# Performance work log

Hardware: AMD Instinct MI355X
Metric: run time of the kernel (lower is better)

Reference implementation:

```python
import jax, jax.numpy as jnp
import numpy as np

D = 1024  # input_size
H = 1024  # hidden_size
B = 128
R = 512


def _lin(x, W, b):
    return x @ W + b


def setup_inputs() -> dict:
    key = jax.random.key(0)
    ks = jax.random.split(key, 20)
    s = 0.02
    inp = {
        "V": jax.random.normal(ks[0], (B, R, D), jnp.float32),
        "s_t": jax.random.normal(ks[1], (B, D), jnp.float32),
        "h_t": jax.random.normal(ks[2], (B, D), jnp.float32),
        # weights stored [in, out] (y = x @ W + b)
        "Wv": jax.random.normal(ks[3], (D, H), jnp.float32) * s,
        "bv": jnp.zeros((H,), jnp.float32),
        "Wsp": jax.random.normal(ks[4], (D, D), jnp.float32) * s,
        "bsp": jnp.zeros((D,), jnp.float32),
        "Wsa": jax.random.normal(ks[5], (D, H), jnp.float32) * s,
        "bsa": jnp.zeros((H,), jnp.float32),
        "Whp": jax.random.normal(ks[6], (D, D), jnp.float32) * s,
        "bhp": jnp.zeros((D,), jnp.float32),
        "Wha": jax.random.normal(ks[7], (D, H), jnp.float32) * s,
        "bha": jnp.zeros((H,), jnp.float32),
        "Wal": jax.random.normal(ks[8], (H, 1), jnp.float32) * s,
        "bal": jnp.zeros((1,), jnp.float32),
        "Wcp": jax.random.normal(ks[9], (D, D), jnp.float32) * s,
        "bcp": jnp.zeros((D,), jnp.float32),
    }
    return inp


def reference(V, s_t, h_t, Wv, bv, Wsp, bsp, Wsa, bsa, Whp, bhp, Wha, bha, Wal, bal, Wcp, bcp):
    v_embed = jax.nn.relu(_lin(V, Wv, bv))           # [B,R,H]
    s_proj = jax.nn.relu(_lin(s_t, Wsp, bsp))        # [B,D]
    s_att = _lin(s_proj, Wsa, bsa)                   # [B,H]
    h_proj = jnp.tanh(_lin(h_t, Whp, bhp))           # [B,D]
    h_att = _lin(h_proj, Wha, bha)                   # [B,H]
    regions = jnp.concatenate([V, s_proj[:, None, :]], axis=1)           # [B,R+1,D]
    regions_att = jnp.concatenate([v_embed, s_att[:, None, :]], axis=1)  # [B,R+1,H]
    alpha_input = jnp.tanh(regions_att + h_att[:, None, :])              # [B,R+1,H]
    scores = (_lin(alpha_input, Wal, bal)).squeeze(-1)                   # [B,R+1]
    alpha = jax.nn.softmax(scores, axis=1)                               # [B,R+1]
    context = jnp.einsum("br,brd->bd", alpha, regions)                   # [B,D]
    z_t = jnp.tanh(_lin(context + h_proj, Wcp, bcp))                     # [B,D]
    return z_t
```

## Files before the change

kernel.cpp:

```cpp
#include <hip/hip_runtime.h>


typedef __bf16 bf16x8 __attribute__((ext_vector_type(8)));
typedef float floatx4 __attribute__((ext_vector_type(4)));

__device__ __forceinline__ float tanh_fast(float x) {
    x = fminf(10.0f, fmaxf(-10.0f, x));
    float e = exp2f(x * 2.885390081777927f);
    return (e - 1.0f) * __builtin_amdgcn_rcpf(e + 1.0f);
}

__global__ __launch_bounds__(256) void wvt_kernel(
    const float* __restrict__ Wv, __bf16* __restrict__ WvT) {
    __shared__ float tile[64][65];
    const int k0 = blockIdx.x * 64, n0 = blockIdx.y * 64;
    const int c = threadIdx.x & 63, r = threadIdx.x >> 6;
#pragma unroll
    for (int i = 0; i < 16; ++i)
        tile[r + i * 4][c] = Wv[(size_t)(k0 + r + i * 4) * 1024 + n0 + c];
    __syncthreads();
#pragma unroll
    for (int i = 0; i < 16; ++i)
        WvT[(size_t)(n0 + r + i * 4) * 1024 + k0 + c] =
            (__bf16)tile[c][r + i * 4];
}

__global__ __launch_bounds__(512) void small_gemm_k(
    const float* __restrict__ A0, const float* __restrict__ W0,
    const float* __restrict__ b0, float* __restrict__ C0, int act0,
    const float* __restrict__ A1, const float* __restrict__ W1,
    const float* __restrict__ b1, float* __restrict__ C1, int act1) {
    const float* A; const float* W; const float* bs; float* C; int act;
    if (blockIdx.z == 0) { A = A0; W = W0; bs = b0; C = C0; act = act0; }
    else                 { A = A1; W = W1; bs = b1; C = C1; act = act1; }
    __shared__ float red[3][8][128];
    const int tid = threadIdx.x;
    const int nl = tid & 127, kq = tid >> 7;
    const int n = blockIdx.x * 128 + nl;
    const int m0 = blockIdx.y * 8;
    const float* Ab = A + m0 * 1024;
    float acc[8] = {};
    const int kbeg = kq * 256, kend = kbeg + 256;
#pragma unroll 4
    for (int k = kbeg; k < kend; ++k) {
        float w = W[(size_t)k * 1024 + n];
#pragma unroll
        for (int mi = 0; mi < 8; ++mi)
            acc[mi] = fmaf(Ab[mi * 1024 + k], w, acc[mi]);
    }
    if (kq > 0) {
#pragma unroll
        for (int mi = 0; mi < 8; ++mi) red[kq - 1][mi][nl] = acc[mi];
    }
    __syncthreads();
    if (kq == 0) {
        float bias = bs[n];
#pragma unroll
        for (int mi = 0; mi < 8; ++mi) {
            float v = acc[mi] + red[0][mi][nl] + red[1][mi][nl] +
                      red[2][mi][nl] + bias;
            if (act == 1) v = fmaxf(v, 0.0f);
            else if (act == 2) v = tanh_fast(v);
            C[(size_t)(m0 + mi) * 1024 + n] = v;
        }
    }
}

__global__ __launch_bounds__(256, 3) void score_gemm_k(
    const float* __restrict__ V, const __bf16* __restrict__ WvT,
    const float* __restrict__ bv, const float* __restrict__ h_att,
    const float* __restrict__ Wal, float* __restrict__ scores) {
    __shared__ __bf16 As[2][128 * 40];
    __shared__ __bf16 Bs[2][128 * 32];

    const int tid = threadIdx.x;
    const int bid = blockIdx.x;
    const int xcd = bid & 7;
    const int j = bid >> 3;
    const int mtile = xcd * 64 + (j >> 3);
    const int ntile = j & 7;
    const int m0 = mtile * 128, n0 = ntile * 128;
    const int wid = tid >> 6, lane = tid & 63;
    const int wm = wid & 1, wn = wid >> 1;
    const int lcol = lane & 15, quad = lane >> 4;

    floatx4 acc[4][4] = {};

    const int am = tid >> 1;
    const int ak = (tid & 1) * 16;
    const float* aptr = V + (size_t)(m0 + am) * 1024 + ak;

    const int g0n = tid >> 2, g0ks = tid & 3;
    const int g1n = (256 + tid) >> 2, g1ks = tid & 3;
    const int g0kg = g0ks ^ ((g0n >> 1) & 3);
    const int g1kg = g1ks ^ ((g1n >> 1) & 3);
    const __bf16* bp0 = WvT + (size_t)(n0 + g0n) * 1024 + g0kg * 8;
    const __bf16* bp1 = WvT + (size_t)(n0 + g1n) * 1024 + g1kg * 8;

    auto stage_A = [&](int buf, float4 f0, float4 f1, float4 f2, float4 f3) {
        bf16x8 u0, u1;
        u0[0] = (__bf16)f0.x; u0[1] = (__bf16)f0.y;
        u0[2] = (__bf16)f0.z; u0[3] = (__bf16)f0.w;
        u0[4] = (__bf16)f1.x; u0[5] = (__bf16)f1.y;
        u0[6] = (__bf16)f1.z; u0[7] = (__bf16)f1.w;
        u1[0] = (__bf16)f2.x; u1[1] = (__bf16)f2.y;
        u1[2] = (__bf16)f2.z; u1[3] = (__bf16)f2.w;
        u1[4] = (__bf16)f3.x; u1[5] = (__bf16)f3.y;
        u1[6] = (__bf16)f3.z; u1[7] = (__bf16)f3.w;
        __bf16* awr = &As[buf][am * 40 + ak];
        *reinterpret_cast<bf16x8*>(awr) = u0;
        *reinterpret_cast<bf16x8*>(awr + 8) = u1;
    };
    auto dma_B = [&](int buf, int k0) {
        __builtin_amdgcn_global_load_lds(
            (const __attribute__((address_space(1))) void*)(bp0 + k0),
            (__attribute__((address_space(3))) void*)(&Bs[buf][tid * 8]),
            16, 0, 0);
        __builtin_amdgcn_global_load_lds(
            (const __attribute__((address_space(1))) void*)(bp1 + k0),
            (__attribute__((address_space(3))) void*)(&Bs[buf][(256 + tid) * 8]),
            16, 0, 0);
    };

    dma_B(0, 0);
    {
        const float4* fp = reinterpret_cast<const float4*>(aptr);
        stage_A(0, fp[0], fp[1], fp[2], fp[3]);
    }
    __syncthreads();

    for (int kk = 0; kk < 32; ++kk) {
        const int cur = kk & 1, nxt = cur ^ 1;
        float4 f0, f1, f2, f3;
        const bool pf = (kk < 31);
        if (pf) {
            dma_B(nxt, (kk + 1) * 32);
            const float4* fp =
                reinterpret_cast<const float4*>(aptr + (kk + 1) * 32);
            f0 = fp[0]; f1 = fp[1]; f2 = fp[2]; f3 = fp[3];
        }
        bf16x8 af[4], bfr[4];
#pragma unroll
        for (int mi = 0; mi < 4; ++mi)
            af[mi] = *reinterpret_cast<const bf16x8*>(
                &As[cur][(wm * 64 + mi * 16 + lcol) * 40 + quad * 8]);
#pragma unroll
        for (int ni = 0; ni < 4; ++ni) {
            int n = wn * 64 + ni * 16 + lcol;
            int ks = quad ^ ((n >> 1) & 3);
            bfr[ni] = *reinterpret_cast<const bf16x8*>(
                &Bs[cur][n * 32 + ks * 8]);
        }
#pragma unroll
        for (int mi = 0; mi < 4; ++mi)
#pragma unroll
            for (int ni = 0; ni < 4; ++ni)
                acc[mi][ni] = __builtin_amdgcn_mfma_f32_16x16x32_bf16(
                    af[mi], bfr[ni], acc[mi][ni], 0, 0, 0);
        if (pf) stage_A(nxt, f0, f1, f2, f3);
        __syncthreads();
    }

    const int b = m0 >> 9;
    float wal[4], hat[4], bvv[4];
#pragma unroll
    for (int ni = 0; ni < 4; ++ni) {
        int n = n0 + wn * 64 + ni * 16 + lcol;
        wal[ni] = Wal[n];
        hat[ni] = h_att[b * 1024 + n];
        bvv[ni] = bv[n];
    }
    float p[16];
#pragma unroll
    for (int mi = 0; mi < 4; ++mi) {
#pragma unroll
        for (int rg = 0; rg < 4; ++rg) {
            float s = 0.f;
#pragma unroll
            for (int ni = 0; ni < 4; ++ni) {
                float x = acc[mi][ni][rg] + bvv[ni];
                x = fmaxf(x, 0.f);
                s = fmaf(wal[ni], tanh_fast(x + hat[ni]), s);
            }
            p[mi * 4 + rg] = s;
        }
    }
#pragma unroll
    for (int off = 1; off < 16; off <<= 1) {
#pragma unroll
        for (int i = 0; i < 16; ++i) p[i] += __shfl_xor(p[i], off, 64);
    }
    if (lcol == 0) {
#pragma unroll
        for (int mi = 0; mi < 4; ++mi)
#pragma unroll
            for (int rg = 0; rg < 4; ++rg) {
                int row = m0 + wm * 64 + mi * 16 + quad * 4 + rg;
                atomicAdd(&scores[b * 513 + (row & 511)], p[mi * 4 + rg]);
            }
    }
}

__global__ __launch_bounds__(256) void lastrow_k(
    const float* __restrict__ s_att, const float* __restrict__ h_att,
    const float* __restrict__ Wal, float* __restrict__ scores) {
    int b = blockIdx.x, tid = threadIdx.x;
    float s = 0.f;
    for (int h = tid; h < 1024; h += 256)
        s += Wal[h] * tanh_fast(s_att[b * 1024 + h] + h_att[b * 1024 + h]);
#pragma unroll
    for (int off = 32; off >= 1; off >>= 1) s += __shfl_xor(s, off, 64);
    __shared__ float red[4];
    if ((tid & 63) == 0) red[tid >> 6] = s;
    __syncthreads();
    if (tid == 0) scores[b * 513 + 512] = red[0] + red[1] + red[2] + red[3];
}

__global__ __launch_bounds__(256) void softmax_k(
    const float* __restrict__ scores, float* __restrict__ alpha) {
    int b = blockIdx.x, tid = threadIdx.x;
    const float* s = scores + b * 513;
    float v0 = s[tid];
    float v1 = s[tid + 256];
    float v2 = (tid == 0) ? s[512] : -1e30f;
    float m = fmaxf(v0, fmaxf(v1, v2));
#pragma unroll
    for (int off = 32; off >= 1; off >>= 1) m = fmaxf(m, __shfl_xor(m, off, 64));
    __shared__ float red[4];
    int w = tid >> 6;
    if ((tid & 63) == 0) red[w] = m;
    __syncthreads();
    m = fmaxf(fmaxf(red[0], red[1]), fmaxf(red[2], red[3]));
    const float L2E = 1.4426950408889634f;
    float e0 = exp2f((v0 - m) * L2E);
    float e1 = exp2f((v1 - m) * L2E);
    float e2 = (tid == 0) ? exp2f((v2 - m) * L2E) : 0.f;
    float sum = e0 + e1 + e2;
#pragma unroll
    for (int off = 32; off >= 1; off >>= 1) sum += __shfl_xor(sum, off, 64);
    __syncthreads();
    if ((tid & 63) == 0) red[w] = sum;
    __syncthreads();
    sum = red[0] + red[1] + red[2] + red[3];
    float inv = 1.0f / sum;
    float* a = alpha + b * 513;
    a[tid] = e0 * inv;
    a[tid + 256] = e1 * inv;
    if (tid == 0) a[512] = e2 * inv;
}

__global__ __launch_bounds__(256) void ctx_k(
    const float* __restrict__ V, const float* __restrict__ alpha,
    const float* __restrict__ s_proj, const float* __restrict__ h_proj,
    float* __restrict__ ctxsum) {
    const int b = blockIdx.x, dq = blockIdx.y;
    const int tid = threadIdx.x;
    const int dl = tid & 63, rq = tid >> 6;
    __shared__ float sal[513];
    __shared__ float red[3][64][4];
    for (int i = tid; i < 513; i += 256) sal[i] = alpha[b * 513 + i];
    __syncthreads();
    const int d0 = dq * 256 + dl * 4;
    const float* vp = V + ((size_t)b * 512 + rq * 128) * 1024 + d0;
    float a0 = 0, a1 = 0, a2 = 0, a3 = 0;
#pragma unroll 8
    for (int r = 0; r < 128; ++r) {
        float al = sal[rq * 128 + r];
        const float4 vv = *reinterpret_cast<const float4*>(vp + (size_t)r * 1024);
        a0 = fmaf(al, vv.x, a0); a1 = fmaf(al, vv.y, a1);
        a2 = fmaf(al, vv.z, a2); a3 = fmaf(al, vv.w, a3);
    }
    if (rq > 0) {
        red[rq - 1][dl][0] = a0; red[rq - 1][dl][1] = a1;
        red[rq - 1][dl][2] = a2; red[rq - 1][dl][3] = a3;
    }
    __syncthreads();
    if (rq == 0) {
#pragma unroll
        for (int q = 0; q < 3; ++q) {
            a0 += red[q][dl][0]; a1 += red[q][dl][1];
            a2 += red[q][dl][2]; a3 += red[q][dl][3];
        }
        float4 sp = *reinterpret_cast<const float4*>(s_proj + b * 1024 + d0);
        float4 hp = *reinterpret_cast<const float4*>(h_proj + b * 1024 + d0);
        float aR = sal[512];
        float4 o;
        o.x = fmaf(aR, sp.x, a0) + hp.x;
        o.y = fmaf(aR, sp.y, a1) + hp.y;
        o.z = fmaf(aR, sp.z, a2) + hp.z;
        o.w = fmaf(aR, sp.w, a3) + hp.w;
        *reinterpret_cast<float4*>(ctxsum + b * 1024 + d0) = o;
    }
}

extern "C" void kernel_launch(void* const* d_in, const int* in_sizes, int n_in,
                              void* d_out, int out_size, void* d_ws,
                              size_t ws_size, hipStream_t stream) {
    const float* V   = (const float*)d_in[0];
    const float* s_t = (const float*)d_in[1];
    const float* h_t = (const float*)d_in[2];
    const float* Wv  = (const float*)d_in[3];
    const float* bv  = (const float*)d_in[4];
    const float* Wsp = (const float*)d_in[5];
    const float* bsp = (const float*)d_in[6];
    const float* Wsa = (const float*)d_in[7];
    const float* bsa = (const float*)d_in[8];
    const float* Whp = (const float*)d_in[9];
    const float* bhp = (const float*)d_in[10];
    const float* Wha = (const float*)d_in[11];
    const float* bha = (const float*)d_in[12];
    const float* Wal = (const float*)d_in[13];
    const float* Wcp = (const float*)d_in[15];
    const float* bcp = (const float*)d_in[16];
    float* out = (float*)d_out;

    char* ws = (char*)d_ws;
    __bf16* WvT   = (__bf16*)(ws + 0);
    float* s_proj = (float*)(ws + 2097152);
    float* h_proj = (float*)(ws + 2621440);
    float* s_att  = (float*)(ws + 3145728);
    float* h_att  = (float*)(ws + 3670016);
    float* scores = (float*)(ws + 4194304);
    float* alpha  = (float*)(ws + 4456960);
    float* ctxsum = (float*)(ws + 4719616);

    hipLaunchKernelGGL(wvt_kernel, dim3(16, 16), dim3(256), 0, stream, Wv, WvT);
    hipLaunchKernelGGL(small_gemm_k, dim3(8, 16, 2), dim3(512), 0, stream,
                       s_t, Wsp, bsp, s_proj, 1,
                       h_t, Whp, bhp, h_proj, 2);
    hipLaunchKernelGGL(small_gemm_k, dim3(8, 16, 2), dim3(512), 0, stream,
                       s_proj, Wsa, bsa, s_att, 0,
                       h_proj, Wha, bha, h_att, 0);
    (void)hipMemsetAsync(scores, 0, 128 * 513 * sizeof(float), stream);
    hipLaunchKernelGGL(score_gemm_k, dim3(4096), dim3(256), 0, stream,
                       V, WvT, bv, h_att, Wal, scores);
    hipLaunchKernelGGL(lastrow_k, dim3(128), dim3(256), 0, stream,
                       s_att, h_att, Wal, scores);
    hipLaunchKernelGGL(softmax_k, dim3(128), dim3(256), 0, stream,
                       scores, alpha);
    hipLaunchKernelGGL(ctx_k, dim3(128, 4), dim3(256), 0, stream,
                       V, alpha, s_proj, h_proj, ctxsum);
    hipLaunchKernelGGL(small_gemm_k, dim3(8, 16, 1), dim3(512), 0, stream,
                       ctxsum, Wcp, bcp, out, 2,
                       ctxsum, Wcp, bcp, out, 2);
}
```

Baseline: 879.0 us.

## Pre-convert V to bf16 and load GEMM operands directly into registers

When the workspace is large enough, a new kernel converts V to bf16 once. The score GEMM and the context reduction then read the half-size copy. The score GEMM drops its LDS staging and barriers: each wave loads its A and B fragments straight from global memory into double-buffered registers and computes a 128x64 tile. The context sum now accumulates from bf16 V, which lowers precision and adds an extra full pass over V for the conversion. Whether the workspace is big enough to take this path is unknown.

```diff
diff --git a/kernel.cpp b/kernel.cpp
--- a/kernel.cpp
+++ b/kernel.cpp
@@ -2,12 +2,26 @@
 
 
 typedef __bf16 bf16x8 __attribute__((ext_vector_type(8)));
+typedef __bf16 bf16x4 __attribute__((ext_vector_type(4)));
 typedef float floatx4 __attribute__((ext_vector_type(4)));
 
 __device__ __forceinline__ float tanh_fast(float x) {
     x = fminf(10.0f, fmaxf(-10.0f, x));
     float e = exp2f(x * 2.885390081777927f);
     return (e - 1.0f) * __builtin_amdgcn_rcpf(e + 1.0f);
+}
+
+__global__ __launch_bounds__(256) void vbf_k(
+    const float* __restrict__ V, __bf16* __restrict__ Vb) {
+    size_t idx = ((size_t)blockIdx.x * 256 + threadIdx.x) * 8;
+    float4 f0 = *reinterpret_cast<const float4*>(V + idx);
+    float4 f1 = *reinterpret_cast<const float4*>(V + idx + 4);
+    bf16x8 u;
+    u[0] = (__bf16)f0.x; u[1] = (__bf16)f0.y;
+    u[2] = (__bf16)f0.z; u[3] = (__bf16)f0.w;
+    u[4] = (__bf16)f1.x; u[5] = (__bf16)f1.y;
+    u[6] = (__bf16)f1.z; u[7] = (__bf16)f1.w;
+    *reinterpret_cast<bf16x8*>(Vb + idx) = u;
 }
 
 __global__ __launch_bounds__(256) void wvt_kernel(
@@ -66,113 +80,89 @@
     }
 }
 
-__global__ __launch_bounds__(256, 3) void score_gemm_k(
-    const float* __restrict__ V, const __bf16* __restrict__ WvT,
+template <bool ABF16>
+__global__ __launch_bounds__(256, 2) void score2_k(
+    const void* __restrict__ Vv, const __bf16* __restrict__ WvT,
     const float* __restrict__ bv, const float* __restrict__ h_att,
     const float* __restrict__ Wal, float* __restrict__ scores) {
-    __shared__ __bf16 As[2][128 * 40];
-    __shared__ __bf16 Bs[2][128 * 32];
-
     const int tid = threadIdx.x;
-    const int bid = blockIdx.x;
-    const int xcd = bid & 7;
-    const int j = bid >> 3;
-    const int mtile = xcd * 64 + (j >> 3);
-    const int ntile = j & 7;
-    const int m0 = mtile * 128, n0 = ntile * 128;
+    const int bidx = blockIdx.x;
+    const int xcd = bidx & 7;
+    const int i = bidx >> 3;
+    const int nt = i & 3;
+    const int mloc = i >> 2;
+    const int m0 = (xcd * 64 + mloc) * 128;
     const int wid = tid >> 6, lane = tid & 63;
-    const int wm = wid & 1, wn = wid >> 1;
+    const int n0 = nt * 256 + wid * 64;
     const int lcol = lane & 15, quad = lane >> 4;
 
-    floatx4 acc[4][4] = {};
-
-    const int am = tid >> 1;
-    const int ak = (tid & 1) * 16;
-    const float* aptr = V + (size_t)(m0 + am) * 1024 + ak;
-
-    const int g0n = tid >> 2, g0ks = tid & 3;
-    const int g1n = (256 + tid) >> 2, g1ks = tid & 3;
-    const int g0kg = g0ks ^ ((g0n >> 1) & 3);
-    const int g1kg = g1ks ^ ((g1n >> 1) & 3);
-    const __bf16* bp0 = WvT + (size_t)(n0 + g0n) * 1024 + g0kg * 8;
-    const __bf16* bp1 = WvT + (size_t)(n0 + g1n) * 1024 + g1kg * 8;
-
-    auto stage_A = [&](int buf, float4 f0, float4 f1, float4 f2, float4 f3) {
-        bf16x8 u0, u1;
-        u0[0] = (__bf16)f0.x; u0[1] = (__bf16)f0.y;
-        u0[2] = (__bf16)f0.z; u0[3] = (__bf16)f0.w;
-        u0[4] = (__bf16)f1.x; u0[5] = (__bf16)f1.y;
-        u0[6] = (__bf16)f1.z; u0[7] = (__bf16)f1.w;
-        u1[0] = (__bf16)f2.x; u1[1] = (__bf16)f2.y;
-        u1[2] = (__bf16)f2.z; u1[3] = (__bf16)f2.w;
-        u1[4] = (__bf16)f3.x; u1[5] = (__bf16)f3.y;
-        u1[6] = (__bf16)f3.z; u1[7] = (__bf16)f3.w;
-        __bf16* awr = &As[buf][am * 40 + ak];
-        *reinterpret_cast<bf16x8*>(awr) = u0;
-        *reinterpret_cast<bf16x8*>(awr + 8) = u1;
+    floatx4 acc[8][4] = {};
+
+    const int laneoff = lcol * 1024 + quad * 8;
+    const __bf16* Ab = (const __bf16*)Vv + (size_t)m0 * 1024 + laneoff;
+    const float* Af = (const float*)Vv + (size_t)m0 * 1024 + laneoff;
+    const __bf16* Bb = WvT + (size_t)n0 * 1024 + laneoff;
+
+    bf16x8 a[2][8], b[2][4];
+
+    auto loadstep = [&](int buf, int kk) {
+        const int ke = kk * 32;
+        if constexpr (ABF16) {
+#pragma unroll
+            for (int mi = 0; mi < 8; ++mi)
+                a[buf][mi] = *reinterpret_cast<const bf16x8*>(
+                    Ab + mi * 16384 + ke);
+        } else {
+#pragma unroll
+            for (int mi = 0; mi < 8; ++mi) {
+                const float* p = Af + mi * 16384 + ke;
+                float4 f0 = *reinterpret_cast<const float4*>(p);
+                float4 f1 = *reinterpret_cast<const float4*>(p + 4);
+                bf16x8 u;
+                u[0] = (__bf16)f0.x; u[1] = (__bf16)f0.y;
+                u[2] = (__bf16)f0.z; u[3] = (__bf16)f0.w;
+                u[4] = (__bf16)f1.x; u[5] = (__bf16)f1.y;
+                u[6] = (__bf16)f1.z; u[7] = (__bf16)f1.w;
+                a[buf][mi] = u;
+            }
+        }
+#pragma unroll
+        for (int ni = 0; ni < 4; ++ni)
+            b[buf][ni] = *reinterpret_cast<const bf16x8*>(
+                Bb + ni * 16384 + ke);
     };
-    auto dma_B = [&](int buf, int k0) {
-        __builtin_amdgcn_global_load_lds(
-            (const __attribute__((address_space(1))) void*)(bp0 + k0),
-            (__attribute__((address_space(3))) void*)(&Bs[buf][tid * 8]),
-            16, 0, 0);
-        __builtin_amdgcn_global_load_lds(
-            (const __attribute__((address_space(1))) void*)(bp1 + k0),
-            (__attribute__((address_space(3))) void*)(&Bs[buf][(256 + tid) * 8]),
-            16, 0, 0);
-    };
-
-    dma_B(0, 0);
-    {
-        const float4* fp = reinterpret_cast<const float4*>(aptr);
-        stage_A(0, fp[0], fp[1], fp[2], fp[3]);
-    }
-    __syncthreads();
-
-    for (int kk = 0; kk < 32; ++kk) {
-        const int cur = kk & 1, nxt = cur ^ 1;
-        float4 f0, f1, f2, f3;
-        const bool pf = (kk < 31);
-        if (pf) {
-            dma_B(nxt, (kk + 1) * 32);
-            const float4* fp =
-                reinterpret_cast<const float4*>(aptr + (kk + 1) * 32);
-            f0 = fp[0]; f1 = fp[1]; f2 = fp[2]; f3 = fp[3];
-        }
-        bf16x8 af[4], bfr[4];
-#pragma unroll
-        for (int mi = 0; mi < 4; ++mi)
-            af[mi] = *reinterpret_cast<const bf16x8*>(
-                &As[cur][(wm * 64 + mi * 16 + lcol) * 40 + quad * 8]);
-#pragma unroll
-        for (int ni = 0; ni < 4; ++ni) {
-            int n = wn * 64 + ni * 16 + lcol;
-            int ks = quad ^ ((n >> 1) & 3);
-            bfr[ni] = *reinterpret_cast<const bf16x8*>(
-                &Bs[cur][n * 32 + ks * 8]);
-        }
-#pragma unroll
-        for (int mi = 0; mi < 4; ++mi)
+    auto mfmastep = [&](int buf) {
+#pragma unroll
+        for (int mi = 0; mi < 8; ++mi)
 #pragma unroll
             for (int ni = 0; ni < 4; ++ni)
                 acc[mi][ni] = __builtin_amdgcn_mfma_f32_16x16x32_bf16(
-                    af[mi], bfr[ni], acc[mi][ni], 0, 0, 0);
-        if (pf) stage_A(nxt, f0, f1, f2, f3);
-        __syncthreads();
-    }
-
-    const int b = m0 >> 9;
+                    a[buf][mi], b[buf][ni], acc[mi][ni], 0, 0, 0);
+    };
+
+    loadstep(0, 0);
+    for (int kk2 = 0; kk2 < 15; ++kk2) {
+        loadstep(1, 2 * kk2 + 1);
+        mfmastep(0);
+        loadstep(0, 2 * kk2 + 2);
+        mfmastep(1);
+    }
+    loadstep(1, 31);
+    mfmastep(0);
+    mfmastep(1);
+
+    const int b_idx = m0 >> 9;
     float wal[4], hat[4], bvv[4];
 #pragma unroll
     for (int ni = 0; ni < 4; ++ni) {
-        int n = n0 + wn * 64 + ni * 16 + lcol;
+        int n = n0 + ni * 16 + lcol;
         wal[ni] = Wal[n];
-        hat[ni] = h_att[b * 1024 + n];
+        hat[ni] = h_att[b_idx * 1024 + n];
         bvv[ni] = bv[n];
     }
-    float p[16];
-#pragma unroll
-    for (int mi = 0; mi < 4; ++mi) {
+    float p[32];
+#pragma unroll
+    for (int mi = 0; mi < 8; ++mi) {
 #pragma unroll
         for (int rg = 0; rg < 4; ++rg) {
             float s = 0.f;
@@ -188,15 +178,16 @@
 #pragma unroll
     for (int off = 1; off < 16; off <<= 1) {
 #pragma unroll
-        for (int i = 0; i < 16; ++i) p[i] += __shfl_xor(p[i], off, 64);
+        for (int j = 0; j < 32; ++j) p[j] += __shfl_xor(p[j], off, 64);
     }
     if (lcol == 0) {
 #pragma unroll
-        for (int mi = 0; mi < 4; ++mi)
+        for (int mi = 0; mi < 8; ++mi)
 #pragma unroll
             for (int rg = 0; rg < 4; ++rg) {
-                int row = m0 + wm * 64 + mi * 16 + quad * 4 + rg;
-                atomicAdd(&scores[b * 513 + (row & 511)], p[mi * 4 + rg]);
+                int row = m0 + mi * 16 + quad * 4 + rg;
+                atomicAdd(&scores[b_idx * 513 + (row & 511)],
+                          p[mi * 4 + rg]);
             }
     }
 }
@@ -249,8 +240,9 @@
     if (tid == 0) a[512] = e2 * inv;
 }
 
-__global__ __launch_bounds__(256) void ctx_k(
-    const float* __restrict__ V, const float* __restrict__ alpha,
+template <bool VBF>
+__global__ __launch_bounds__(256) void ctx2_k(
+    const void* __restrict__ Vv, const float* __restrict__ alpha,
     const float* __restrict__ s_proj, const float* __restrict__ h_proj,
     float* __restrict__ ctxsum) {
     const int b = blockIdx.x, dq = blockIdx.y;
@@ -261,14 +253,31 @@
     for (int i = tid; i < 513; i += 256) sal[i] = alpha[b * 513 + i];
     __syncthreads();
     const int d0 = dq * 256 + dl * 4;
-    const float* vp = V + ((size_t)b * 512 + rq * 128) * 1024 + d0;
     float a0 = 0, a1 = 0, a2 = 0, a3 = 0;
+    if constexpr (VBF) {
+        const __bf16* vp =
+            (const __bf16*)Vv + ((size_t)b * 512 + rq * 128) * 1024 + d0;
 #pragma unroll 8
-    for (int r = 0; r < 128; ++r) {
-        float al = sal[rq * 128 + r];
-        const float4 vv = *reinterpret_cast<const float4*>(vp + (size_t)r * 1024);
-        a0 = fmaf(al, vv.x, a0); a1 = fmaf(al, vv.y, a1);
-        a2 = fmaf(al, vv.z, a2); a3 = fmaf(al, vv.w, a3);
+        for (int r = 0; r < 128; ++r) {
+            float al = sal[rq * 128 + r];
+            bf16x4 vv =
+                *reinterpret_cast<const bf16x4*>(vp + (size_t)r * 1024);
+            a0 = fmaf(al, (float)vv[0], a0);
+            a1 = fmaf(al, (float)vv[1], a1);
+            a2 = fmaf(al, (float)vv[2], a2);
+            a3 = fmaf(al, (float)vv[3], a3);
+        }
+    } else {
+        const float* vp =
+            (const float*)Vv + ((size_t)b * 512 + rq * 128) * 1024 + d0;
+#pragma unroll 8
+        for (int r = 0; r < 128; ++r) {
+            float al = sal[rq * 128 + r];
+            const float4 vv =
+                *reinterpret_cast<const float4*>(vp + (size_t)r * 1024);
+            a0 = fmaf(al, vv.x, a0); a1 = fmaf(al, vv.y, a1);
+            a2 = fmaf(al, vv.z, a2); a3 = fmaf(al, vv.w, a3);
+        }
     }
     if (rq > 0) {
         red[rq - 1][dl][0] = a0; red[rq - 1][dl][1] = a1;
@@ -314,16 +323,30 @@
     const float* bcp = (const float*)d_in[16];
     float* out = (float*)d_out;
 
+    const size_t VBF_BYTES = 134217728ull;
+    const size_t NEED_BIG = 139461632ull;
+    const bool big = ws_size >= NEED_BIG;
+
     char* ws = (char*)d_ws;
-    __bf16* WvT   = (__bf16*)(ws + 0);
-    float* s_proj = (float*)(ws + 2097152);
-    float* h_proj = (float*)(ws + 2621440);
-    float* s_att  = (float*)(ws + 3145728);
-    float* h_att  = (float*)(ws + 3670016);
-    float* scores = (float*)(ws + 4194304);
-    float* alpha  = (float*)(ws + 4456960);
-    float* ctxsum = (float*)(ws + 4719616);
-
+    __bf16* Vbf; __bf16* WvT; char* base;
+    if (big) {
+        Vbf = (__bf16*)ws;
+        base = ws + VBF_BYTES;
+    } else {
+        Vbf = nullptr;
+        base = ws;
+    }
+    WvT           = (__bf16*)(base);
+    float* s_proj = (float*)(base + 2097152);
+    float* h_proj = (float*)(base + 2621440);
+    float* s_att  = (float*)(base + 3145728);
+    float* h_att  = (float*)(base + 3670016);
+    float* scores = (float*)(base + 4194304);
+    float* alpha  = (float*)(base + 4456960);
+    float* ctxsum = (float*)(base + 4719616);
+
+    if (big)
+        hipLaunchKernelGGL(vbf_k, dim3(32768), dim3(256), 0, stream, V, Vbf);
     hipLaunchKernelGGL(wvt_kernel, dim3(16, 16), dim3(256), 0, stream, Wv, WvT);
     hipLaunchKernelGGL(small_gemm_k, dim3(8, 16, 2), dim3(512), 0, stream,
                        s_t, Wsp, bsp, s_proj, 1,
@@ -332,14 +355,22 @@
                        s_proj, Wsa, bsa, s_att, 0,
                        h_proj, Wha, bha, h_att, 0);
     (void)hipMemsetAsync(scores, 0, 128 * 513 * sizeof(float), stream);
-    hipLaunchKernelGGL(score_gemm_k, dim3(4096), dim3(256), 0, stream,
-                       V, WvT, bv, h_att, Wal, scores);
+    if (big)
+        hipLaunchKernelGGL(score2_k<true>, dim3(2048), dim3(256), 0, stream,
+                           (const void*)Vbf, WvT, bv, h_att, Wal, scores);
+    else
+        hipLaunchKernelGGL(score2_k<false>, dim3(2048), dim3(256), 0, stream,
+                           (const void*)V, WvT, bv, h_att, Wal, scores);
     hipLaunchKernelGGL(lastrow_k, dim3(128), dim3(256), 0, stream,
                        s_att, h_att, Wal, scores);
     hipLaunchKernelGGL(softmax_k, dim3(128), dim3(256), 0, stream,
                        scores, alpha);
-    hipLaunchKernelGGL(ctx_k, dim3(128, 4), dim3(256), 0, stream,
-                       V, alpha, s_proj, h_proj, ctxsum);
+    if (big)
+        hipLaunchKernelGGL(ctx2_k<true>, dim3(128, 4), dim3(256), 0, stream,
+                           (const void*)Vbf, alpha, s_proj, h_proj, ctxsum);
+    else
+        hipLaunchKernelGGL(ctx2_k<false>, dim3(128, 4), dim3(256), 0, stream,
+                           (const void*)V, alpha, s_proj, h_proj, ctxsum);
     hipLaunchKernelGGL(small_gemm_k, dim3(8, 16, 1), dim3(512), 0, stream,
                        ctxsum, Wcp, bcp, out, 2,
                        ctxsum, Wcp, bcp, out, 2);
```

New measurement: 989.8 us. 1.13x slower.
